# Optimization experiments

Hardware: AMD Instinct MI355X
Metric: run time of the kernel (lower is better)

Reference implementation:

```python
import jax, jax.numpy as jnp
import numpy as np
from functools import partial

ENC = 128  # encoding_dim

def setup_inputs() -> dict:
    key = jax.random.key(0)
    ks = jax.random.split(key, 6)
    B, S, E, H = 8, 512, 128, 512
    action_sequence = jax.random.normal(ks[0], (B, S, E), dtype=jnp.float32)
    # nn.Linear-style init scale ~ 1/sqrt(fan_in)
    W1 = jax.random.normal(ks[1], (H, E), dtype=jnp.float32) / np.sqrt(E)
    b1 = jnp.zeros((H,), dtype=jnp.float32)
    W2 = jax.random.normal(ks[2], (ENC * ENC, H), dtype=jnp.float32) / np.sqrt(H)
    b2 = jnp.zeros((ENC * ENC,), dtype=jnp.float32)
    e0 = jax.random.normal(ks[3], (1, ENC), dtype=jnp.float32) / 10.0
    return {"action_sequence": action_sequence, "W1": W1, "b1": b1,
            "W2": W2, "b2": b2, "e0": e0}

def reference(action_sequence, W1, b1, W2, b2, e0):
    B, S, E = action_sequence.shape
    # fast-weight generation: two dense layers
    hidden = jnp.tanh(jnp.einsum('bse,he->bsh', action_sequence, W1) + b1)
    Wa = (jnp.einsum('bsh,oh->bso', hidden, W2) + b2).reshape(B, S, ENC, ENC)
    # attractor dynamics: et_{i} = clamp(et_{i-1} @ Wa[:, i], -5, 5)
    e0b = jnp.broadcast_to(e0, (B, ENC))
    Wa_seq = jnp.transpose(Wa[:, 1:], (1, 0, 2, 3))  # [S-1, B, ENC, ENC]
    def step(et, Wa_i):
        et_next = jnp.clip(jnp.einsum('bd,bde->be', et, Wa_i), -5.0, 5.0)
        return et_next, et_next
    _, es = jax.lax.scan(step, e0b, Wa_seq)  # [S-1, B, ENC]
    encodings = jnp.concatenate([e0b[None], es], axis=0)  # [S, B, ENC]
    return jnp.transpose(encodings, (1, 0, 2))  # [B, S, ENC]
```

## Files before the change

### kernel.cpp

```cpp
#include <hip/hip_runtime.h>
#include <cstddef>

#define BB 8
#define SS 512
#define EE 128
#define HH 512
#define ENC 128

__device__ __forceinline__ float xla_tanhf(float x) {
    const float cx = fminf(fmaxf(x, -9.0f), 9.0f);
    const float x2 = __fmul_rn(cx, cx);
    float p = -2.76076847742355e-16f;
    p = __fadd_rn(__fmul_rn(p, x2), 2.00018790482477e-13f);
    p = __fadd_rn(__fmul_rn(p, x2), -8.60467152213735e-11f);
    p = __fadd_rn(__fmul_rn(p, x2), 5.12229709037114e-08f);
    p = __fadd_rn(__fmul_rn(p, x2), 1.48572235717979e-05f);
    p = __fadd_rn(__fmul_rn(p, x2), 6.37261928875436e-04f);
    p = __fadd_rn(__fmul_rn(p, x2), 4.89352455891786e-03f);
    const float num = __fmul_rn(cx, p);
    float q = 1.19825839466702e-06f;
    q = __fadd_rn(__fmul_rn(q, x2), 1.18534705686654e-04f);
    q = __fadd_rn(__fmul_rn(q, x2), 2.26843463243900e-03f);
    q = __fadd_rn(__fmul_rn(q, x2), 4.89352518554385e-03f);
    const float r = __fdiv_rn(num, q);
    return (fabsf(x) < 0.0004f) ? x : r;
}

__device__ __forceinline__ int arow_map(int m, int chm1, int chsh, int i0) {
    return ((m >> chsh) * SS) + i0 + (m & chm1);
}

template <int ACT, int MAPROW, int TRANSP>
__global__ __launch_bounds__(256) void gemm_nt(const float* __restrict__ A,
                                               const float* __restrict__ Bm,
                                               const float* __restrict__ bias,
                                               float* __restrict__ C,
                                               int N, int K,
                                               int chm1, int chsh, int i0) {
    __shared__ float As[16][132];
    __shared__ float Bs[16][132];

    const int tid = threadIdx.x;
    const int tx = tid & 15;
    const int ty = tid >> 4;
    const int n0 = blockIdx.x * 128;
    const int m0 = blockIdx.y * 128;
    const int bd = blockIdx.x >> 4;
    const int be = blockIdx.x & 15;

    const int lr = tid >> 2;
    const int lc = (tid & 3) << 2;

    const int ga0 = MAPROW ? arow_map(m0 + lr, chm1, chsh, i0) : (m0 + lr);
    const int ga1 = MAPROW ? arow_map(m0 + lr + 64, chm1, chsh, i0) : (m0 + lr + 64);

    const int r0 = lr, r1 = lr + 64;
    const int gb0 = TRANSP ? ((bd * 16 + (r0 >> 3)) * 128 + be * 8 + (r0 & 7))
                           : (n0 + r0);
    const int gb1 = TRANSP ? ((bd * 16 + (r1 >> 3)) * 128 + be * 8 + (r1 & 7))
                           : (n0 + r1);

    float acc[8][8];
#pragma unroll
    for (int i = 0; i < 8; ++i)
#pragma unroll
        for (int j = 0; j < 8; ++j) acc[i][j] = 0.f;

    for (int k0 = 0; k0 < K; k0 += 16) {
        const float4 a0 = *(const float4*)(A + (size_t)ga0 * K + (k0 + lc));
        const float4 a1 = *(const float4*)(A + (size_t)ga1 * K + (k0 + lc));
        const float4 b0 = *(const float4*)(Bm + (size_t)gb0 * K + (k0 + lc));
        const float4 b1 = *(const float4*)(Bm + (size_t)gb1 * K + (k0 + lc));

        __syncthreads();

        As[lc + 0][lr] = a0.x; As[lc + 1][lr] = a0.y;
        As[lc + 2][lr] = a0.z; As[lc + 3][lr] = a0.w;
        As[lc + 0][lr + 64] = a1.x; As[lc + 1][lr + 64] = a1.y;
        As[lc + 2][lr + 64] = a1.z; As[lc + 3][lr + 64] = a1.w;
        Bs[lc + 0][lr] = b0.x; Bs[lc + 1][lr] = b0.y;
        Bs[lc + 2][lr] = b0.z; Bs[lc + 3][lr] = b0.w;
        Bs[lc + 0][lr + 64] = b1.x; Bs[lc + 1][lr + 64] = b1.y;
        Bs[lc + 2][lr + 64] = b1.z; Bs[lc + 3][lr + 64] = b1.w;

        __syncthreads();

#pragma unroll
        for (int k = 0; k < 16; ++k) {
            const float4 av0 = *(const float4*)&As[k][ty * 8];
            const float4 av1 = *(const float4*)&As[k][ty * 8 + 4];
            const float4 bv0 = *(const float4*)&Bs[k][tx * 4];
            const float4 bv1 = *(const float4*)&Bs[k][64 + tx * 4];
            const float a[8] = {av0.x, av0.y, av0.z, av0.w, av1.x, av1.y, av1.z, av1.w};
            const float b[8] = {bv0.x, bv0.y, bv0.z, bv0.w, bv1.x, bv1.y, bv1.z, bv1.w};
#pragma unroll
            for (int i = 0; i < 8; ++i)
#pragma unroll
                for (int j = 0; j < 8; ++j)
                    acc[i][j] = __fadd_rn(acc[i][j], __fmul_rn(a[i], b[j]));
        }
    }

#pragma unroll
    for (int i = 0; i < 8; ++i) {
        const int m = m0 + ty * 8 + i;
        if (TRANSP) {
#pragma unroll
            for (int j = 0; j < 8; ++j) {
                const int c = (j < 4) ? (tx * 4 + j) : (64 + tx * 4 + (j - 4));
                const int d = bd * 16 + (c >> 3);
                const int ee = be * 8 + (c & 7);
                const int o = d * 128 + ee;
                const float v = __fadd_rn(acc[i][j], bias[o]);
                C[(size_t)m * N + ((size_t)(d >> 2) * 128 + ee) * 4 + (d & 3)] = v;
            }
        } else {
            float v[8];
#pragma unroll
            for (int j = 0; j < 4; ++j) {
                const int n = n0 + tx * 4 + j;
                v[j] = __fadd_rn(acc[i][j], bias[n]);
                if (ACT) v[j] = xla_tanhf(v[j]);
            }
#pragma unroll
            for (int j = 4; j < 8; ++j) {
                const int n = n0 + 64 + tx * 4 + (j - 4);
                v[j] = __fadd_rn(acc[i][j], bias[n]);
                if (ACT) v[j] = xla_tanhf(v[j]);
            }
            *(float4*)(C + (size_t)m * N + (n0 + tx * 4)) =
                make_float4(v[0], v[1], v[2], v[3]);
            *(float4*)(C + (size_t)m * N + (n0 + 64 + tx * 4)) =
                make_float4(v[4], v[5], v[6], v[7]);
        }
    }
}

__device__ __forceinline__ void scan_barrier_nodrain() {
    asm volatile("s_waitcnt lgkmcnt(0)" ::: "memory");
    __builtin_amdgcn_s_barrier();
    asm volatile("" ::: "memory");
}

#define SCAN_QUARTER(Q, WC, WP)                                             \
    {                                                                       \
                                                             \
        const int pf = (ii - start) * 4 + (Q) + 3;                          \
        const int pfc = (pf < nq) ? pf : (nq - 1);      \
        const float4* P4 = Wb4 + (size_t)(start + (pfc >> 2)) * 4096        \
                               + (size_t)(pfc & 3) * 1024 + e;              \
        _Pragma("unroll")                                                   \
        for (int u = 0; u < 8; ++u) WP[u] = P4[u * 128];                    \
        asm volatile("" ::: "memory");                                      \
              \
        _Pragma("unroll")                                                   \
        for (int dq = 0; dq < 8; ++dq) {                                    \
            const float4 t4 = *(const float4*)&et[s][(Q) * 32 + dq * 4];    \
            const float4 wv = WC[dq];        \
            sum = __fadd_rn(sum, __fmul_rn(t4.x, wv.x));                    \
            sum = __fadd_rn(sum, __fmul_rn(t4.y, wv.y));                    \
            sum = __fadd_rn(sum, __fmul_rn(t4.z, wv.z));                    \
            sum = __fadd_rn(sum, __fmul_rn(t4.w, wv.w));                    \
        }                                                                   \
    }

__global__ __launch_bounds__(128, 1) void scan_kernel(const float* __restrict__ Wa,
                                                      const float* __restrict__ e0,
                                                      float* __restrict__ et_state,
                                                      float* __restrict__ out,
                                                      int i0, int CH) {
    __shared__ float et[2][128];
    const int b = blockIdx.x;
    const int e = threadIdx.x;

    int s = 0;
    if (i0 == 0) {
        const float v = e0[e];
        et[0][e] = v;
        out[(size_t)b * SS * ENC + e] = v;
    } else {
        et[0][e] = et_state[b * 128 + e];
    }
    __syncthreads();

    const int start = (i0 == 0) ? 1 : 0;
    const float4* Wb4 = (const float4*)(Wa + (size_t)b * CH * (ENC * ENC));
    const int nq = (CH - start) * 4;

    float4 w0[8], w1[8], w2[8], w3[8];

    {
        const float4* S4 = Wb4 + (size_t)start * 4096 + e;
#pragma unroll
        for (int u = 0; u < 8; ++u) w0[u] = S4[u * 128];
#pragma unroll
        for (int u = 0; u < 8; ++u) w1[u] = S4[(8 + u) * 128];
#pragma unroll
        for (int u = 0; u < 8; ++u) w2[u] = S4[(16 + u) * 128];
    }
    asm volatile("" ::: "memory");

    for (int ii = start; ii < CH; ++ii) {
        float sum = 0.f;
        SCAN_QUARTER(0, w0, w3)
        SCAN_QUARTER(1, w1, w0)
        SCAN_QUARTER(2, w2, w1)
        SCAN_QUARTER(3, w3, w2)
        const float v = fminf(fmaxf(sum, -5.f), 5.f);
        out[((size_t)b * SS + (i0 + ii)) * ENC + e] = v;
        et[s ^ 1][e] = v;
        scan_barrier_nodrain();
        s ^= 1;
    }
    et_state[b * 128 + e] = et[s][e];
}

extern "C" void kernel_launch(void* const* d_in, const int* in_sizes, int n_in,
                              void* d_out, int out_size, void* d_ws, size_t ws_size,
                              hipStream_t stream) {
    const float* A  = (const float*)d_in[0];
    const float* W1 = (const float*)d_in[1];
    const float* b1 = (const float*)d_in[2];
    const float* W2 = (const float*)d_in[3];
    const float* b2 = (const float*)d_in[4];
    const float* e0 = (const float*)d_in[5];
    float* out = (float*)d_out;

    int CH = 16;
    for (int c = 512; c >= 16; c >>= 1) {
        const size_t Mc = (size_t)BB * c;
        const size_t need = 4096 + Mc * HH * sizeof(float) +
                            Mc * (size_t)(ENC * ENC) * sizeof(float);
        if (need <= ws_size) { CH = c; break; }
    }
    const int Mc = BB * CH;
    int chsh = 0;
    while ((1 << chsh) < CH) ++chsh;
    const int chm1 = CH - 1;

    float* et_state = (float*)d_ws;
    float* hidden   = (float*)((char*)d_ws + 4096);
    float* Wa       = hidden + (size_t)Mc * HH;

    for (int i0 = 0; i0 < SS; i0 += CH) {
        dim3 g1(HH / 128, Mc / 128);
        gemm_nt<1, 1, 0><<<g1, 256, 0, stream>>>(A, W1, b1, hidden, HH, EE,
                                                 chm1, chsh, i0);
        dim3 g2((ENC * ENC) / 128, Mc / 128);
        gemm_nt<0, 0, 1><<<g2, 256, 0, stream>>>(hidden, W2, b2, Wa, ENC * ENC,
                                                 HH, 0, 0, 0);
        scan_kernel<<<BB, 128, 0, stream>>>(Wa, e0, et_state, out, i0, CH);
    }
}
```

Measured before the change: 1.394 ms.

## Split scan into producer/consumer waves with LDS double-buffered weight prefetch

Replaces the register-prefetch scan with a 256-thread block. Two producer waves stream the next step's 64KB Wa matrix into a double-buffered LDS region using global_load_lds, while two consumer waves compute the matvec from the current LDS buffer. The aim is to hide global memory latency behind compute in the serial recurrence. In exchange it uses about 128KB of LDS per block and adds a full block barrier each step. The producer's vmcnt wait also sits on the critical path of every step.

```diff
diff --git a/kernel.cpp b/kernel.cpp
--- a/kernel.cpp
+++ b/kernel.cpp
@@ -136,83 +136,92 @@
     }
 }
 
-__device__ __forceinline__ void scan_barrier_nodrain() {
-    asm volatile("s_waitcnt lgkmcnt(0)" ::: "memory");
-    __builtin_amdgcn_s_barrier();
-    asm volatile("" ::: "memory");
-}
-
-#define SCAN_QUARTER(Q, WC, WP)                                             \
-    {                                                                       \
-                                                             \
-        const int pf = (ii - start) * 4 + (Q) + 3;                          \
-        const int pfc = (pf < nq) ? pf : (nq - 1);      \
-        const float4* P4 = Wb4 + (size_t)(start + (pfc >> 2)) * 4096        \
-                               + (size_t)(pfc & 3) * 1024 + e;              \
-        _Pragma("unroll")                                                   \
-        for (int u = 0; u < 8; ++u) WP[u] = P4[u * 128];                    \
-        asm volatile("" ::: "memory");                                      \
-              \
-        _Pragma("unroll")                                                   \
-        for (int dq = 0; dq < 8; ++dq) {                                    \
-            const float4 t4 = *(const float4*)&et[s][(Q) * 32 + dq * 4];    \
-            const float4 wv = WC[dq];        \
-            sum = __fadd_rn(sum, __fmul_rn(t4.x, wv.x));                    \
-            sum = __fadd_rn(sum, __fmul_rn(t4.y, wv.y));                    \
-            sum = __fadd_rn(sum, __fmul_rn(t4.z, wv.z));                    \
-            sum = __fadd_rn(sum, __fmul_rn(t4.w, wv.w));                    \
-        }                                                                   \
-    }
-
-__global__ __launch_bounds__(128, 1) void scan_kernel(const float* __restrict__ Wa,
-                                                      const float* __restrict__ e0,
-                                                      float* __restrict__ et_state,
-                                                      float* __restrict__ out,
-                                                      int i0, int CH) {
-    __shared__ float et[2][128];
+#define GLD_LDS16(G, L)                                                     \
+    __builtin_amdgcn_global_load_lds(                                       \
+        (const __attribute__((address_space(1))) void*)(G),                 \
+        (__attribute__((address_space(3))) void*)(L), 16, 0, 0)
+
+__global__ __launch_bounds__(256, 1) void scan_pc(const float* __restrict__ Wa,
+                                                  const float* __restrict__ e0,
+                                                  float* __restrict__ et_state,
+                                                  float* __restrict__ out,
+                                                  int i0, int CH) {
+    __shared__ float W0f[16384];
+    __shared__ float W1f[16384];
+    __shared__ float etb[256];
+
     const int b = blockIdx.x;
-    const int e = threadIdx.x;
-
-    int s = 0;
-    if (i0 == 0) {
-        const float v = e0[e];
-        et[0][e] = v;
-        out[(size_t)b * SS * ENC + e] = v;
-    } else {
-        et[0][e] = et_state[b * 128 + e];
-    }
-    __syncthreads();
-
+    const int tid = threadIdx.x;
     const int start = (i0 == 0) ? 1 : 0;
     const float4* Wb4 = (const float4*)(Wa + (size_t)b * CH * (ENC * ENC));
-    const int nq = (CH - start) * 4;
-
-    float4 w0[8], w1[8], w2[8], w3[8];
-
-    {
-        const float4* S4 = Wb4 + (size_t)start * 4096 + e;
-#pragma unroll
-        for (int u = 0; u < 8; ++u) w0[u] = S4[u * 128];
-#pragma unroll
-        for (int u = 0; u < 8; ++u) w1[u] = S4[(8 + u) * 128];
-#pragma unroll
-        for (int u = 0; u < 8; ++u) w2[u] = S4[(16 + u) * 128];
-    }
-    asm volatile("" ::: "memory");
-
+
+    if (tid < 128) {
+        const int e = tid;
+        if (i0 == 0) {
+            const float v = e0[e];
+            etb[e] = v;
+            out[(size_t)b * SS * ENC + e] = v;
+        } else {
+            etb[e] = et_state[b * 128 + e];
+        }
+    } else {
+        const int w = (tid >> 6) & 1;
+        const int lane = tid & 63;
+        const float4* src = Wb4 + (size_t)start * 4096;
+#pragma unroll
+        for (int k = 0; k < 32; ++k) {
+            const int seg = w * 32 + k;
+            GLD_LDS16(src + seg * 64 + lane, W0f + seg * 256);
+        }
+        asm volatile("s_waitcnt vmcnt(0)" ::: "memory");
+    }
+    __syncthreads();
+
+    int s = 0;
     for (int ii = start; ii < CH; ++ii) {
-        float sum = 0.f;
-        SCAN_QUARTER(0, w0, w3)
-        SCAN_QUARTER(1, w1, w0)
-        SCAN_QUARTER(2, w2, w1)
-        SCAN_QUARTER(3, w3, w2)
-        const float v = fminf(fmaxf(sum, -5.f), 5.f);
-        out[((size_t)b * SS + (i0 + ii)) * ENC + e] = v;
-        et[s ^ 1][e] = v;
-        scan_barrier_nodrain();
+        if (tid < 128) {
+            const int e = tid;
+            const float* Wc = s ? W1f : W0f;
+            const float* etc = etb + s * 128;
+            float sum = 0.f;
+#pragma unroll
+            for (int q = 0; q < 4; ++q) {
+                float4 wv[8];
+#pragma unroll
+                for (int u = 0; u < 8; ++u)
+                    wv[u] = *(const float4*)&Wc[(q * 1024 + u * 128 + e) * 4];
+#pragma unroll
+                for (int u = 0; u < 8; ++u) {
+                    const float4 t4 = *(const float4*)&etc[q * 32 + u * 4];
+                    const float4 x = wv[u];
+                    sum = __fadd_rn(sum, __fmul_rn(t4.x, x.x));
+                    sum = __fadd_rn(sum, __fmul_rn(t4.y, x.y));
+                    sum = __fadd_rn(sum, __fmul_rn(t4.z, x.z));
+                    sum = __fadd_rn(sum, __fmul_rn(t4.w, x.w));
+                }
+            }
+            const float v = fminf(fmaxf(sum, -5.f), 5.f);
+            out[((size_t)b * SS + (i0 + ii)) * ENC + e] = v;
+            etb[(s ^ 1) * 128 + e] = v;
+            asm volatile("s_waitcnt lgkmcnt(0)" ::: "memory");
+        } else {
+            const int w = (tid >> 6) & 1;
+            const int lane = tid & 63;
+            const int nxt = (ii + 1 < CH) ? (ii + 1) : (CH - 1);
+            const float4* src = Wb4 + (size_t)nxt * 4096;
+            float* Wn = s ? W0f : W1f;
+#pragma unroll
+            for (int k = 0; k < 32; ++k) {
+                const int seg = w * 32 + k;
+                GLD_LDS16(src + seg * 64 + lane, Wn + seg * 256);
+            }
+            asm volatile("s_waitcnt vmcnt(0)" ::: "memory");
+        }
+        __builtin_amdgcn_s_barrier();
+        asm volatile("" ::: "memory");
         s ^= 1;
     }
-    et_state[b * 128 + e] = et[s][e];
+    if (tid < 128) et_state[b * 128 + tid] = etb[s * 128 + tid];
 }
 
 extern "C" void kernel_launch(void* const* d_in, const int* in_sizes, int n_in,
@@ -249,6 +258,6 @@
         dim3 g2((ENC * ENC) / 128, Mc / 128);
         gemm_nt<0, 0, 1><<<g2, 256, 0, stream>>>(hidden, W2, b2, Wa, ENC * ENC,
                                                  HH, 0, 0, 0);
-        scan_kernel<<<BB, 128, 0, stream>>>(Wa, e0, et_state, out, i0, CH);
-    }
-}
+        scan_pc<<<BB, 256, 0, stream>>>(Wa, e0, et_state, out, i0, CH);
+    }
+}
```

Result: slower. 1.452 ms (+4.1%).
